# Kernel tuning notes

Measured on AMD Instinct MI355X. Metric: run time of the kernel, lower is better.

The kernel has to match this reference:

```python
import jax, jax.numpy as jnp
import numpy as np

VOCAB, EMB, SEQ, BATCH, LABELS = 50000, 256, 512, 64, 10
H = EMB  # hidden_size = embedding_size


def _lstm(x, Wx, Wh, b, reverse=False):
    # x: [B, T, E] -> last hidden state [B, H]
    B = x.shape[0]
    xt = jnp.swapaxes(x, 0, 1)  # [T, B, E]
    if reverse:
        xt = xt[::-1]
    # precompute input projections for all timesteps: [T, B, 4H]
    zx = jnp.einsum('tbe,eg->tbg', xt, Wx) + b

    def step(carry, z_in):
        h, c = carry
        z = z_in + h @ Wh  # [B, 4H]
        i, f, g, o = jnp.split(z, 4, axis=-1)
        i = jax.nn.sigmoid(i)
        f = jax.nn.sigmoid(f)
        g = jnp.tanh(g)
        o = jax.nn.sigmoid(o)
        c = f * c + i * g
        h = o * jnp.tanh(c)
        return (h, c), None

    init = (jnp.zeros((B, H), x.dtype), jnp.zeros((B, H), x.dtype))
    (h, c), _ = jax.lax.scan(step, init, zx)
    return h


def setup_inputs() -> dict:
    key = jax.random.key(0)
    ks = jax.random.split(key, 10)
    s_emb = 1.0 / np.sqrt(EMB)
    inp = {
        'tokens': jax.random.randint(ks[0], (BATCH, SEQ), 0, VOCAB, dtype=jnp.int32),
        'emb_table': jax.random.normal(ks[1], (VOCAB, EMB), jnp.float32) * 0.05,
        'Wx_f': jax.random.normal(ks[2], (EMB, 4 * H), jnp.float32) * s_emb,
        'Wh_f': jax.random.normal(ks[3], (H, 4 * H), jnp.float32) * s_emb,
        'b_f': jnp.zeros((4 * H,), jnp.float32),
        'Wx_b': jax.random.normal(ks[4], (EMB, 4 * H), jnp.float32) * s_emb,
        'Wh_b': jax.random.normal(ks[5], (H, 4 * H), jnp.float32) * s_emb,
        'b_b': jnp.zeros((4 * H,), jnp.float32),
        'W_out': jax.random.normal(ks[6], (2 * H, LABELS), jnp.float32) * (1.0 / np.sqrt(2 * H)),
        'b_out': jnp.zeros((LABELS,), jnp.float32),
    }
    return inp


def reference(tokens, emb_table, Wx_f, Wh_f, b_f, Wx_b, Wh_b, b_b, W_out, b_out):
    embedded = emb_table[tokens]  # [B, T, E]
    h_fwd = _lstm(embedded, Wx_f, Wh_f, b_f, reverse=False)  # [B, H]
    h_bwd = _lstm(embedded, Wx_b, Wh_b, b_b, reverse=True)   # [B, H]
    feat = jnp.concatenate([h_fwd, h_bwd], axis=-1)  # [B, 2H]
    # dropout is identity in inference mode
    logits = feat @ W_out + b_out
    return jax.nn.softmax(logits, axis=-1)
```

## Files before the change

### kernel.cpp

```cpp
#include <hip/hip_runtime.h>
#include <stdint.h>
#include <stddef.h>


typedef __attribute__((ext_vector_type(8))) short   short8;
typedef __attribute__((ext_vector_type(4))) float   f32x4;
typedef __attribute__((ext_vector_type(4))) unsigned short ushort4v;
typedef __attribute__((ext_vector_type(4))) unsigned int   uint4v;
typedef __attribute__((ext_vector_type(2))) unsigned int   uint2v;

#define EMB16_OFF ((size_t)0)
#define WXT_OFF   ((size_t)25600000)
#define WHT_OFF   ((size_t)26648576)
#define HBUF_OFF  ((size_t)27697152)
#define WS_NEED   ((size_t)28221568)

__device__ __forceinline__ unsigned short f2bf(float f) {
  unsigned int u = __builtin_bit_cast(unsigned int, f);
  u += 0x7fffu + ((u >> 16) & 1u);
  return (unsigned short)(u >> 16);
}
__device__ __forceinline__ float bf2f(unsigned short b) {
  unsigned int u = ((unsigned int)b) << 16;
  return __builtin_bit_cast(float, u);
}
__device__ __forceinline__ float sigf(float x) { return 1.0f / (1.0f + __expf(-x)); }
__device__ __forceinline__ float tanhf_(float x) {
  float t = __expf(-2.0f * fabsf(x));
  float r = (1.0f - t) / (1.0f + t);
  return copysignf(r, x);
}

__global__ __launch_bounds__(256) void k0_transpose(
    const float* __restrict__ wxf, const float* __restrict__ wxb,
    const float* __restrict__ whf, const float* __restrict__ whb,
    unsigned short* __restrict__ wxt, unsigned short* __restrict__ wht) {
  __shared__ float lds[32][33];
  int mat = blockIdx.z;
  const float* src = (mat == 0) ? wxf : (mat == 1) ? wxb : (mat == 2) ? whf : whb;
  unsigned short* dst = (mat == 0) ? wxt : (mat == 1) ? (wxt + 262144)
                      : (mat == 2) ? wht : (wht + 262144);
  int k0 = blockIdx.x * 32;
  int n0 = blockIdx.y * 32;
  int tx = threadIdx.x & 31, ty = threadIdx.x >> 5;
#pragma unroll
  for (int r = 0; r < 4; r++) {
    int k = ty + r * 8;
    lds[k][tx] = src[(size_t)(k0 + k) * 1024 + n0 + tx];
  }
  __syncthreads();
#pragma unroll
  for (int r = 0; r < 4; r++) {
    int n = ty + r * 8;
    dst[(size_t)(n0 + n) * 256 + k0 + tx] = f2bf(lds[tx][n]);
  }
}

__global__ __launch_bounds__(256) void k0b_embcast(
    const float* __restrict__ emb, unsigned short* __restrict__ embbf) {
  size_t i = ((size_t)blockIdx.x * 256 + threadIdx.x) * 8;
  f32x4 v0 = *(const f32x4*)(emb + i);
  f32x4 v1 = *(const f32x4*)(emb + i + 4);
  short8 st;
#pragma unroll
  for (int j = 0; j < 4; j++) {
    st[j]     = (short)f2bf(v0[j]);
    st[4 + j] = (short)f2bf(v1[j]);
  }
  *(short8*)(embbf + i) = st;
}

__global__ __launch_bounds__(256, 1) void k2_rnn(
    const int* __restrict__ tokens, const unsigned short* __restrict__ embbf,
    const unsigned short* __restrict__ wxt,
    const unsigned short* __restrict__ wht,
    const float* __restrict__ bf_, const float* __restrict__ bb_,
    unsigned int* __restrict__ hbufw) {
  int bx = blockIdx.x;
  int tid = threadIdx.x;
  int w = tid >> 6, lane = tid & 63, q = lane >> 4, l16 = lane & 15;

  unsigned int* desc = hbufw + 131072;
  {
    unsigned int xcc = __builtin_amdgcn_s_getreg((31 << 11) | 20) & 0xffu;
    if (tid == 0) {
      unsigned int v = 0x100u | xcc;
      asm volatile("global_store_dword %0, %1, off sc1"
                   :: "v"(desc + bx), "v"(v) : "memory");
    }
  }
  int g, cg;
  {
    const unsigned int* dp = desc + (lane & 31);
    unsigned int dv;
    while (true) {
      asm volatile("global_load_dword %0, %1, off sc1\n\ts_waitcnt vmcnt(0)"
                   : "=&v"(dv) : "v"(dp) : "memory");
      if (__all((dv & 0x100u) != 0u)) break;
    }
    unsigned int key = ((dv & 0xffu) << 8) | (unsigned int)(lane & 31);
    int rank = 0;
#pragma unroll
    for (int j = 0; j < 32; ++j) {
      unsigned int kj = __shfl(key, j);
      rank += (kj < key) ? 1 : 0;
    }
    int myrank = __shfl(rank, bx);
    g  = myrank >> 2;
    cg = myrank & 3;
  }
  int d  = g >> 2;
  int rg = g & 3;

  __shared__ unsigned short wx2[32][256][8];
  __shared__ unsigned short hl[2][32][16][8];

  const unsigned short* wxd = wxt + (size_t)d * 262144;
  for (int it = 0; it < 32; ++it) {
    int idx = it * 256 + tid;
    int cl = idx & 255, ch = idx >> 8;
    int gcol = (cl >> 6) * 256 + cg * 64 + (cl & 63);
    *(short8*)(&wx2[ch][cl][0]) = *(const short8*)(wxd + (size_t)gcol * 256 + ch * 8);
  }

  const unsigned short* whd = wht + (size_t)d * 262144;
  short8 bfr[4][8];
#pragma unroll
  for (int cs = 0; cs < 4; cs++) {
    const unsigned short* wp = whd + (size_t)(cs * 256 + cg * 64 + w * 16 + l16) * 256;
#pragma unroll
    for (int kt = 0; kt < 8; kt++)
      bfr[cs][kt] = *(const short8*)(wp + kt * 32 + q * 8);
  }

  {
    unsigned int* hlw = (unsigned int*)&hl[0][0][0][0];
    for (int i = tid; i < 4096; i += 256) hlw[i] = 0;
  }
  __syncthreads();

  const float* bias = d ? bb_ : bf_;
  float bv[4];
#pragma unroll
  for (int cs = 0; cs < 4; cs++) bv[cs] = bias[cs * 256 + cg * 64 + w * 16 + l16];

  float cst[4] = {0.f, 0.f, 0.f, 0.f};
  unsigned int* hb = hbufw + (size_t)g * 8192;
  int prow = w * 4 + q;
  int ps   = lane & 15;
  int rcg0 = (cg + 1) & 3, rcg1 = (cg + 2) & 3, rcg2 = (cg + 3) & 3;
  int pbase = prow * 256 + ps * 4;
  int srow  = (q * 4) * 256 + cg * 64 + w * 16 + l16;
  const int* tokrow = tokens + (rg * 16 + l16) * 512;

  int limit = 16;

  short8 ea[8];
  {
    int ts0 = d ? 511 : 0;
    int tok0 = tokrow[ts0];
    const unsigned short* er = embbf + (size_t)tok0 * 256 + q * 8;
#pragma unroll
    for (int kt = 0; kt < 8; ++kt) ea[kt] = *(const short8*)(er + kt * 32);
  }

  for (int t = 0; t < 512; ++t) {
    int buf = t & 1;
    int tsn = (t < 511) ? (d ? 510 - t : t + 1) : 0;
    int tok_n = tokrow[tsn];

    f32x4 acc[4];
#pragma unroll
    for (int cs = 0; cs < 4; ++cs) acc[cs] = {0.f, 0.f, 0.f, 0.f};
#pragma unroll
    for (int kt = 0; kt < 8; ++kt) {
#pragma unroll
      for (int cs = 0; cs < 4; ++cs) {
        short8 xb = *(const short8*)(&wx2[kt * 4 + q][cs * 64 + w * 16 + l16][0]);
        acc[cs] = __builtin_amdgcn_mfma_f32_16x16x32_bf16(ea[kt], xb, acc[cs], 0, 0, 0);
      }
    }

    const unsigned int* q0 = hb + buf * 4096 + pbase + rcg0 * 64;
    const unsigned int* q1 = hb + buf * 4096 + pbase + rcg1 * 64;
    const unsigned int* q2 = hb + buf * 4096 + pbase + rcg2 * 64;
    unsigned int tg = (unsigned int)t << 16;
    uint4v r0, r1, r2;
    bool got = false;
    for (int it = 0; it < limit; ++it) {
      asm volatile(
          "global_load_dwordx4 %[r0], %[p0], off sc0\n\t"
          "global_load_dwordx4 %[r1], %[p1], off sc0\n\t"
          "global_load_dwordx4 %[r2], %[p2], off sc0\n\t"
          "s_waitcnt vmcnt(0)"
          : [r0] "=&v"(r0), [r1] "=&v"(r1), [r2] "=&v"(r2)
          : [p0] "v"(q0), [p1] "v"(q1), [p2] "v"(q2)
          : "memory");
      unsigned int bad = (r0[0] ^ tg) | (r0[1] ^ tg) | (r0[2] ^ tg) | (r0[3] ^ tg)
                       | (r1[0] ^ tg) | (r1[1] ^ tg) | (r1[2] ^ tg) | (r1[3] ^ tg)
                       | (r2[0] ^ tg) | (r2[1] ^ tg) | (r2[2] ^ tg) | (r2[3] ^ tg);
      if (__all((bad & 0xffff0000u) == 0)) { got = true; break; }
    }
    if (!got) {
      limit >>= 1;
      const unsigned int* m0 = q0 + 65536;
      const unsigned int* m1 = q1 + 65536;
      const unsigned int* m2 = q2 + 65536;
      while (true) {
        asm volatile(
            "global_load_dwordx4 %[r0], %[p0], off sc1\n\t"
            "global_load_dwordx4 %[r1], %[p1], off sc1\n\t"
            "global_load_dwordx4 %[r2], %[p2], off sc1\n\t"
            "s_waitcnt vmcnt(0)"
            : [r0] "=&v"(r0), [r1] "=&v"(r1), [r2] "=&v"(r2)
            : [p0] "v"(m0), [p1] "v"(m1), [p2] "v"(m2)
            : "memory");
        unsigned int bad = (r0[0] ^ tg) | (r0[1] ^ tg) | (r0[2] ^ tg) | (r0[3] ^ tg)
                         | (r1[0] ^ tg) | (r1[1] ^ tg) | (r1[2] ^ tg) | (r1[3] ^ tg)
                         | (r2[0] ^ tg) | (r2[1] ^ tg) | (r2[2] ^ tg) | (r2[3] ^ tg);
        if (__all((bad & 0xffff0000u) == 0)) break;
      }
    }

    short8 ean[8];
    {
      const unsigned short* ern = embbf + (size_t)tok_n * 256 + q * 8;
#pragma unroll
      for (int kt = 0; kt < 8; ++kt) ean[kt] = *(const short8*)(ern + kt * 32);
    }

    {
      int e4 = (ps & 1) * 4, ch2 = ps >> 1;
      uint2v w0, w1, w2;
      w0[0] = __builtin_amdgcn_perm(r0[1], r0[0], 0x05040100u);
      w0[1] = __builtin_amdgcn_perm(r0[3], r0[2], 0x05040100u);
      w1[0] = __builtin_amdgcn_perm(r1[1], r1[0], 0x05040100u);
      w1[1] = __builtin_amdgcn_perm(r1[3], r1[2], 0x05040100u);
      w2[0] = __builtin_amdgcn_perm(r2[1], r2[0], 0x05040100u);
      w2[1] = __builtin_amdgcn_perm(r2[3], r2[2], 0x05040100u);
      *(uint2v*)(&hl[buf][rcg0 * 8 + ch2][prow][e4]) = w0;
      *(uint2v*)(&hl[buf][rcg1 * 8 + ch2][prow][e4]) = w1;
      *(uint2v*)(&hl[buf][rcg2 * 8 + ch2][prow][e4]) = w2;
    }
    __syncthreads();

#pragma unroll
    for (int kt = 0; kt < 8; ++kt) {
      short8 ha = *(const short8*)(&hl[buf][kt * 4 + q][l16][0]);
#pragma unroll
      for (int cs = 0; cs < 4; ++cs)
        acc[cs] = __builtin_amdgcn_mfma_f32_16x16x32_bf16(ha, bfr[cs][kt], acc[cs], 0, 0, 0);
    }

    unsigned int* hwn = hb + ((buf ^ 1) * 4096) + srow;
    unsigned int wtag = ((unsigned int)(t + 1)) << 16;
    int dim = cg * 64 + w * 16 + l16;
    int chO = dim >> 3, eO = dim & 7;
    unsigned int sw[4];
#pragma unroll
    for (int r = 0; r < 4; ++r) {
      float iv = sigf(acc[0][r] + bv[0]);
      float fv = sigf(acc[1][r] + bv[1]);
      float gv = tanhf_(acc[2][r] + bv[2]);
      float ov = sigf(acc[3][r] + bv[3]);
      cst[r] = fv * cst[r] + iv * gv;
      float hv = ov * tanhf_(cst[r]);
      unsigned short h16 = f2bf(hv);
      sw[r] = wtag | (unsigned int)h16;
      hl[buf ^ 1][chO][q * 4 + r][eO] = h16;
    }
    {
      unsigned int* hwm = hwn + 65536;
      asm volatile(
          "global_store_dword %[p], %[v0], off sc0\n\t"
          "global_store_dword %[p], %[v1], off offset:1024 sc0\n\t"
          "global_store_dword %[p], %[v2], off offset:2048 sc0\n\t"
          "global_store_dword %[p], %[v3], off offset:3072 sc0\n\t"
          "global_store_dword %[m], %[v0], off sc1\n\t"
          "global_store_dword %[m], %[v1], off offset:1024 sc1\n\t"
          "global_store_dword %[m], %[v2], off offset:2048 sc1\n\t"
          "global_store_dword %[m], %[v3], off offset:3072 sc1"
          :: [p] "v"(hwn), [m] "v"(hwm), [v0] "v"(sw[0]), [v1] "v"(sw[1]),
             [v2] "v"(sw[2]), [v3] "v"(sw[3])
          : "memory");
    }

#pragma unroll
    for (int kt = 0; kt < 8; ++kt) ea[kt] = ean[kt];
  }
}

__global__ __launch_bounds__(64) void k3_out(
    const unsigned int* __restrict__ hbufw,
    const float* __restrict__ wout, const float* __restrict__ bout,
    float* __restrict__ out) {
  int b = blockIdx.x, tid = threadIdx.x;
  int rg = b >> 4, r = b & 15;
  const unsigned int* hf  = hbufw + (size_t)rg * 8192 + r * 256;
  const unsigned int* hbk = hbufw + 32768 + (size_t)rg * 8192 + r * 256;
  float p[10];
#pragma unroll
  for (int l = 0; l < 10; l++) p[l] = 0.f;
  for (int k = tid; k < 512; k += 64) {
    unsigned int wd = (k < 256) ? hf[k] : hbk[k - 256];
    float f = bf2f((unsigned short)(wd & 0xffffu));
    const float* wr = wout + k * 10;
#pragma unroll
    for (int l = 0; l < 10; l++) p[l] += f * wr[l];
  }
#pragma unroll
  for (int off = 32; off; off >>= 1)
#pragma unroll
    for (int l = 0; l < 10; l++) p[l] += __shfl_down(p[l], off);
  if (tid == 0) {
    float lg[10], m = -1e30f;
#pragma unroll
    for (int l = 0; l < 10; l++) { lg[l] = p[l] + bout[l]; m = fmaxf(m, lg[l]); }
    float sum = 0.f;
#pragma unroll
    for (int l = 0; l < 10; l++) { lg[l] = __expf(lg[l] - m); sum += lg[l]; }
    float inv = 1.0f / sum;
#pragma unroll
    for (int l = 0; l < 10; l++) out[b * 10 + l] = lg[l] * inv;
  }
}

extern "C" void kernel_launch(void* const* d_in, const int* in_sizes, int n_in,
                              void* d_out, int out_size, void* d_ws, size_t ws_size,
                              hipStream_t stream) {
  const int*   tokens = (const int*)d_in[0];
  const float* emb    = (const float*)d_in[1];
  const float* wxf    = (const float*)d_in[2];
  const float* whf    = (const float*)d_in[3];
  const float* bf_    = (const float*)d_in[4];
  const float* wxb    = (const float*)d_in[5];
  const float* whb    = (const float*)d_in[6];
  const float* bb_    = (const float*)d_in[7];
  const float* wout   = (const float*)d_in[8];
  const float* bout   = (const float*)d_in[9];
  float* out = (float*)d_out;

  char* ws = (char*)d_ws;
  unsigned short* embbf = (unsigned short*)(ws + EMB16_OFF);
  unsigned short* wxt   = (unsigned short*)(ws + WXT_OFF);
  unsigned short* wht   = (unsigned short*)(ws + WHT_OFF);
  unsigned int*   hbufw = (unsigned int*)(ws + HBUF_OFF);
  (void)ws_size; (void)in_sizes; (void)n_in; (void)out_size;

  hipMemsetAsync(ws + HBUF_OFF, 0, 524416, stream);

  k0_transpose<<<dim3(8, 32, 4), 256, 0, stream>>>(wxf, wxb, whf, whb, wxt, wht);
  k0b_embcast<<<6250, 256, 0, stream>>>(emb, embbf);
  k2_rnn<<<32, 256, 0, stream>>>(tokens, embbf, wxt, wht, bf_, bb_, hbufw);
  k3_out<<<64, 64, 0, stream>>>(hbufw, wout, bout, out);
}
```

Baseline: 1.428 ms.

## Split remote hidden-state polling across three waves with sleep backoff

Changes the cross-block h exchange so that only waves 0-2 each poll one remote column group, using four contiguous 16-byte loads per lane. Previously every wave polled three groups with scattered loads. This cuts redundant polling traffic and the number of distinct addresses per spin, and adds s_sleep backoff between retries. It also inserts a vmcnt wait between the sc0 and sc1 mirror stores, which orders them but adds latency on the store path.

```diff
diff --git a/kernel.cpp b/kernel.cpp
--- a/kernel.cpp
+++ b/kernel.cpp
@@ -146,12 +146,13 @@
 
   float cst[4] = {0.f, 0.f, 0.f, 0.f};
   unsigned int* hb = hbufw + (size_t)g * 8192;
-  int prow = w * 4 + q;
-  int ps   = lane & 15;
-  int rcg0 = (cg + 1) & 3, rcg1 = (cg + 2) & 3, rcg2 = (cg + 3) & 3;
-  int pbase = prow * 256 + ps * 4;
   int srow  = (q * 4) * 256 + cg * 64 + w * 16 + l16;
   const int* tokrow = tokens + (rg * 16 + l16) * 512;
+
+  int p_w   = (cg + 1 + w) & 3;
+  int prow2 = lane >> 2;
+  int pq4   = lane & 3;
+  int pbase2 = prow2 * 256 + p_w * 64 + pq4 * 16;
 
   int limit = 16;
 
@@ -181,44 +182,62 @@
       }
     }
 
-    const unsigned int* q0 = hb + buf * 4096 + pbase + rcg0 * 64;
-    const unsigned int* q1 = hb + buf * 4096 + pbase + rcg1 * 64;
-    const unsigned int* q2 = hb + buf * 4096 + pbase + rcg2 * 64;
     unsigned int tg = (unsigned int)t << 16;
-    uint4v r0, r1, r2;
-    bool got = false;
-    for (int it = 0; it < limit; ++it) {
-      asm volatile(
-          "global_load_dwordx4 %[r0], %[p0], off sc0\n\t"
-          "global_load_dwordx4 %[r1], %[p1], off sc0\n\t"
-          "global_load_dwordx4 %[r2], %[p2], off sc0\n\t"
-          "s_waitcnt vmcnt(0)"
-          : [r0] "=&v"(r0), [r1] "=&v"(r1), [r2] "=&v"(r2)
-          : [p0] "v"(q0), [p1] "v"(q1), [p2] "v"(q2)
-          : "memory");
-      unsigned int bad = (r0[0] ^ tg) | (r0[1] ^ tg) | (r0[2] ^ tg) | (r0[3] ^ tg)
-                       | (r1[0] ^ tg) | (r1[1] ^ tg) | (r1[2] ^ tg) | (r1[3] ^ tg)
-                       | (r2[0] ^ tg) | (r2[1] ^ tg) | (r2[2] ^ tg) | (r2[3] ^ tg);
-      if (__all((bad & 0xffff0000u) == 0)) { got = true; break; }
-    }
-    if (!got) {
-      limit >>= 1;
-      const unsigned int* m0 = q0 + 65536;
-      const unsigned int* m1 = q1 + 65536;
-      const unsigned int* m2 = q2 + 65536;
-      while (true) {
+    if (w < 3) {
+      const unsigned int* qp = hb + buf * 4096 + pbase2;
+      uint4v s0, s1, s2, s3;
+      bool got = false;
+      for (int it = 0; it < limit; ++it) {
         asm volatile(
-            "global_load_dwordx4 %[r0], %[p0], off sc1\n\t"
-            "global_load_dwordx4 %[r1], %[p1], off sc1\n\t"
-            "global_load_dwordx4 %[r2], %[p2], off sc1\n\t"
+            "global_load_dwordx4 %[s0], %[pp], off sc0\n\t"
+            "global_load_dwordx4 %[s1], %[pp], off offset:16 sc0\n\t"
+            "global_load_dwordx4 %[s2], %[pp], off offset:32 sc0\n\t"
+            "global_load_dwordx4 %[s3], %[pp], off offset:48 sc0\n\t"
             "s_waitcnt vmcnt(0)"
-            : [r0] "=&v"(r0), [r1] "=&v"(r1), [r2] "=&v"(r2)
-            : [p0] "v"(m0), [p1] "v"(m1), [p2] "v"(m2)
+            : [s0] "=&v"(s0), [s1] "=&v"(s1), [s2] "=&v"(s2), [s3] "=&v"(s3)
+            : [pp] "v"(qp)
             : "memory");
-        unsigned int bad = (r0[0] ^ tg) | (r0[1] ^ tg) | (r0[2] ^ tg) | (r0[3] ^ tg)
-                         | (r1[0] ^ tg) | (r1[1] ^ tg) | (r1[2] ^ tg) | (r1[3] ^ tg)
-                         | (r2[0] ^ tg) | (r2[1] ^ tg) | (r2[2] ^ tg) | (r2[3] ^ tg);
-        if (__all((bad & 0xffff0000u) == 0)) break;
+        unsigned int bad = (s0[0] ^ tg) | (s0[1] ^ tg) | (s0[2] ^ tg) | (s0[3] ^ tg)
+                         | (s1[0] ^ tg) | (s1[1] ^ tg) | (s1[2] ^ tg) | (s1[3] ^ tg)
+                         | (s2[0] ^ tg) | (s2[1] ^ tg) | (s2[2] ^ tg) | (s2[3] ^ tg)
+                         | (s3[0] ^ tg) | (s3[1] ^ tg) | (s3[2] ^ tg) | (s3[3] ^ tg);
+        if (__all((bad & 0xffff0000u) == 0)) { got = true; break; }
+        __builtin_amdgcn_s_sleep(2);
+      }
+      if (!got) {
+        limit >>= 1;
+        const unsigned int* mp = qp + 65536;
+        while (true) {
+          asm volatile(
+              "global_load_dwordx4 %[s0], %[pp], off sc1\n\t"
+              "global_load_dwordx4 %[s1], %[pp], off offset:16 sc1\n\t"
+              "global_load_dwordx4 %[s2], %[pp], off offset:32 sc1\n\t"
+              "global_load_dwordx4 %[s3], %[pp], off offset:48 sc1\n\t"
+              "s_waitcnt vmcnt(0)"
+              : [s0] "=&v"(s0), [s1] "=&v"(s1), [s2] "=&v"(s2), [s3] "=&v"(s3)
+              : [pp] "v"(mp)
+              : "memory");
+          unsigned int bad = (s0[0] ^ tg) | (s0[1] ^ tg) | (s0[2] ^ tg) | (s0[3] ^ tg)
+                           | (s1[0] ^ tg) | (s1[1] ^ tg) | (s1[2] ^ tg) | (s1[3] ^ tg)
+                           | (s2[0] ^ tg) | (s2[1] ^ tg) | (s2[2] ^ tg) | (s2[3] ^ tg)
+                           | (s3[0] ^ tg) | (s3[1] ^ tg) | (s3[2] ^ tg) | (s3[3] ^ tg);
+          if (__all((bad & 0xffff0000u) == 0)) break;
+          __builtin_amdgcn_s_sleep(4);
+        }
+      }
+      {
+        uint4v d0, d1;
+        d0[0] = __builtin_amdgcn_perm(s0[1], s0[0], 0x05040100u);
+        d0[1] = __builtin_amdgcn_perm(s0[3], s0[2], 0x05040100u);
+        d0[2] = __builtin_amdgcn_perm(s1[1], s1[0], 0x05040100u);
+        d0[3] = __builtin_amdgcn_perm(s1[3], s1[2], 0x05040100u);
+        d1[0] = __builtin_amdgcn_perm(s2[1], s2[0], 0x05040100u);
+        d1[1] = __builtin_amdgcn_perm(s2[3], s2[2], 0x05040100u);
+        d1[2] = __builtin_amdgcn_perm(s3[1], s3[0], 0x05040100u);
+        d1[3] = __builtin_amdgcn_perm(s3[3], s3[2], 0x05040100u);
+        int ch0 = p_w * 8 + pq4 * 2;
+        *(uint4v*)(&hl[buf][ch0][prow2][0])     = d0;
+        *(uint4v*)(&hl[buf][ch0 + 1][prow2][0]) = d1;
       }
     }
 
@@ -229,19 +248,6 @@
       for (int kt = 0; kt < 8; ++kt) ean[kt] = *(const short8*)(ern + kt * 32);
     }
 
-    {
-      int e4 = (ps & 1) * 4, ch2 = ps >> 1;
-      uint2v w0, w1, w2;
-      w0[0] = __builtin_amdgcn_perm(r0[1], r0[0], 0x05040100u);
-      w0[1] = __builtin_amdgcn_perm(r0[3], r0[2], 0x05040100u);
-      w1[0] = __builtin_amdgcn_perm(r1[1], r1[0], 0x05040100u);
-      w1[1] = __builtin_amdgcn_perm(r1[3], r1[2], 0x05040100u);
-      w2[0] = __builtin_amdgcn_perm(r2[1], r2[0], 0x05040100u);
-      w2[1] = __builtin_amdgcn_perm(r2[3], r2[2], 0x05040100u);
-      *(uint2v*)(&hl[buf][rcg0 * 8 + ch2][prow][e4]) = w0;
-      *(uint2v*)(&hl[buf][rcg1 * 8 + ch2][prow][e4]) = w1;
-      *(uint2v*)(&hl[buf][rcg2 * 8 + ch2][prow][e4]) = w2;
-    }
     __syncthreads();
 
 #pragma unroll
@@ -276,6 +282,7 @@
           "global_store_dword %[p], %[v1], off offset:1024 sc0\n\t"
           "global_store_dword %[p], %[v2], off offset:2048 sc0\n\t"
           "global_store_dword %[p], %[v3], off offset:3072 sc0\n\t"
+          "s_waitcnt vmcnt(0)\n\t"
           "global_store_dword %[m], %[v0], off sc1\n\t"
           "global_store_dword %[m], %[v1], off offset:1024 sc1\n\t"
           "global_store_dword %[m], %[v2], off offset:2048 sc1\n\t"
```

Measured after the change: 1.378 ms. -3.5%, faster.
